# Optimization experiments

Measured on AMD Instinct MI355X. Metric: run time of the kernel, lower is better.

## Reference

```python
import math
import jax, jax.numpy as jnp
import numpy as np

B, C_IN, C_OUT, D_LATENT, H, W, K = 16, 512, 512, 512, 64, 64, 3
EPS = 1e-8


def setup_inputs() -> dict:
    key = jax.random.key(0)
    ks = jax.random.split(key, 6)
    return {
        "x": jax.random.normal(ks[0], (B, C_IN, H, W), dtype=jnp.float32),
        "w": jax.random.normal(ks[1], (B, D_LATENT), dtype=jnp.float32),
        "noise": jax.random.normal(ks[2], (B, 1, H, W), dtype=jnp.float32),
        "style_w": jax.random.normal(ks[3], (C_IN, D_LATENT), dtype=jnp.float32),
        "style_b": jnp.ones((C_IN,), dtype=jnp.float32),  # bias=1.0 in to_style
        "conv_w": jax.random.normal(ks[4], (C_OUT, C_IN, K, K), dtype=jnp.float32),
        "scale_noise": jax.random.normal(ks[5], (1,), dtype=jnp.float32),
        "bias": jnp.zeros((C_OUT,), dtype=jnp.float32),
    }


def reference(x, w, noise, style_w, style_b, conv_w, scale_noise, bias):
    b, c, h, ww = x.shape
    o, _, k, _ = conv_w.shape
    # EqualizedLinear to_style: runtime_coef = 1/sqrt(d_latent), lr_mul=1
    lin_coef = 1.0 / math.sqrt(style_w.shape[1])
    style = w @ (style_w * lin_coef).T + style_b  # [B, C_in]
    # EqualizedWeight for conv: runtime_coef = 1/sqrt(C_in*K*K)
    conv_coef = 1.0 / math.sqrt(c * k * k)
    weights = (conv_w * conv_coef)[None] * style[:, None, :, None, None]  # [B,O,I,K,K]
    # demodulate
    sigma_inv = jax.lax.rsqrt(jnp.sum(weights * weights, axis=(2, 3, 4), keepdims=True) + EPS)
    weights = weights * sigma_inv
    # grouped conv: groups = batch
    xg = x.reshape(1, b * c, h, ww)
    wg = weights.reshape(b * o, c, k, k)
    y = jax.lax.conv_general_dilated(
        xg, wg, window_strides=(1, 1), padding="SAME",
        feature_group_count=b,
        dimension_numbers=("NCHW", "OIHW", "NCHW"))
    y = y.reshape(b, o, h, ww)
    y = y + scale_noise[None, :, None, None] * noise
    return jax.nn.leaky_relu(y + bias[None, :, None, None], negative_slope=0.2)
```

## Files before the change

kernel.cpp:

```cpp
#include <hip/hip_runtime.h>
#include <hip/hip_bf16.h>


#define B_    16
#define CIN   512
#define COUT  512
#define DLAT  512
#define H_    64
#define W_    64

constexpr float LIN_COEF  = 0.04419417382415922f;
constexpr float CONV_COEF = 0.014731391274719739f;

typedef __attribute__((ext_vector_type(8))) short short8;
typedef __attribute__((ext_vector_type(4))) float f32x4;

__device__ __forceinline__ void gl2lds16(const void* g, void* l) {
  __builtin_amdgcn_global_load_lds(
      (const __attribute__((address_space(1))) unsigned*)g,
      (__attribute__((address_space(3))) unsigned*)l, 16, 0, 0);
}

__global__ __launch_bounds__(256) void pre1(
    const float* __restrict__ w, const float* __restrict__ style_w,
    const float* __restrict__ style_b, const float* __restrict__ conv_w,
    float* __restrict__ style, float* __restrict__ wsq,
    __hip_bfloat16* __restrict__ wtp2, __hip_bfloat16* __restrict__ xt) {
  __shared__ float lw[CIN * 9];
  const int bid = blockIdx.x, tid = threadIdx.x;
  if (bid < 2048) {
    int gw = bid * 4 + (tid >> 6), lane = tid & 63;
    int b = gw >> 9, c = gw & 511;
    const float* wp = w + b * DLAT;
    const float* sw = style_w + c * DLAT;
    float v = 0.f;
    for (int d = lane; d < DLAT; d += 64) v = fmaf(wp[d], sw[d], v);
    #pragma unroll
    for (int off = 32; off > 0; off >>= 1) v += __shfl_down(v, off, 64);
    if (lane == 0) style[b * CIN + c] = fmaf(v, LIN_COEF, style_b[c]);
  } else if (bid < 3072) {
    int idx = (bid - 2048) * 256 + tid;
    const float* p = conv_w + (size_t)idx * 9;
    float s = 0.f;
    #pragma unroll
    for (int t = 0; t < 9; ++t) s = fmaf(p[t], p[t], s);
    wsq[idx] = s;
  } else if (bid < 3584) {
    int o = bid - 3072;
    for (int j = tid; j < CIN * 9; j += 256) lw[j] = conv_w[(size_t)o * (CIN * 9) + j];
    __syncthreads();
    for (int g = tid; g < 576; g += 256) {
      int chunk = g / 36, rem = g - chunk * 36, pos = rem >> 2, kqq = rem & 3;
      short8 v;
      #pragma unroll
      for (int e = 0; e < 8; ++e) {
        int ic = chunk * 32 + kqq * 8 + e;
        ((__hip_bfloat16*)&v)[e] = __float2bfloat16(lw[ic * 9 + pos]);
      }
      ((short8*)wtp2)[(size_t)g * 512 + o] = v;
    }
  } else {
    int idx = bid - 3584;
    int b = idx / 260, pb = idx - b * 260;
    int hh, ww;
    if (pb < 66)       { hh = 0;  ww = pb; }
    else if (pb < 132) { hh = 65; ww = pb - 66; }
    else if (pb < 196) { hh = pb - 132 + 1; ww = 0; }
    else               { hh = pb - 196 + 1; ww = 65; }
    unsigned* p = (unsigned*)(xt + (((size_t)b * 66 + hh) * 66 + ww) * CIN);
    p[tid] = 0u;
  }
}

#define LSTR 136
__global__ __launch_bounds__(256) void pre2(
    const float* __restrict__ x, const float* __restrict__ style,
    const float* __restrict__ wsq, float* __restrict__ scale_bo,
    __hip_bfloat16* __restrict__ xt) {
  __shared__ __align__(16) char sm2[64 * LSTR * 2];
  const int bid = blockIdx.x, tid = threadIdx.x;
  if (bid < 2048) {
    int gw = bid * 4 + (tid >> 6), lane = tid & 63;
    int b = gw >> 9, o = gw & 511;
    const float* st = style + b * CIN;
    const float* wq = wsq + o * CIN;
    float v = 0.f;
    for (int i = lane; i < CIN; i += 64) { float s = st[i]; v = fmaf(s * s, wq[i], v); }
    #pragma unroll
    for (int off = 32; off > 0; off >>= 1) v += __shfl_down(v, off, 64);
    if (lane == 0)
      scale_bo[b * COUT + o] = CONV_COEF * rsqrtf(fmaf(CONV_COEF * CONV_COEF, v, 1e-8f));
  } else {
    int idx = bid - 2048;
    int b = idx >> 8, rem = idx & 255, h = rem >> 2, ic0 = (rem & 3) * 128;
    __hip_bfloat16* ls = (__hip_bfloat16*)sm2;
    for (int j = tid; j < 128 * 64; j += 256) {
      int i = j >> 6, ww = j & 63;
      float v = x[(((size_t)b * CIN + ic0 + i) * H_ + h) * W_ + ww] * style[b * CIN + ic0 + i];
      ls[ww * LSTR + i] = __float2bfloat16(v);
    }
    __syncthreads();
    for (int j = tid; j < 64 * 16; j += 256) {
      int ww = j >> 4, part = j & 15;
      __hip_bfloat16* dst = xt + (((size_t)b * 66 + h + 1) * 66 + (ww + 1)) * CIN + ic0 + part * 8;
      *(short8*)dst = *(const short8*)(ls + ww * LSTR + part * 8);
    }
  }
}

__global__ __launch_bounds__(256, 3) void conv_mfma(
    const __hip_bfloat16* __restrict__ xt, const __hip_bfloat16* __restrict__ wtp2,
    const float* __restrict__ scale_bo, const float* __restrict__ noise,
    const float* __restrict__ scale_noise, const float* __restrict__ bias,
    float* __restrict__ out) {
  __shared__ __align__(16) char smem[25344];

  const int tid = threadIdx.x, lane = tid & 63, wid = tid >> 6;
  const int mrow = lane & 15, kq = lane >> 4;
  const int b  = blockIdx.x >> 4;
  const int h0 = (blockIdx.x & 15) << 2;
  const int o0 = blockIdx.y << 6;
  const int h  = h0 + wid;

  const size_t xbase = ((size_t)(b * 66 + h0)) * (66 * 512);
  int xoff[7];
  #pragma unroll
  for (int i = 0; i < 7; ++i) {
    int slot = wid + i * 4;
    int t = slot * 64 + lane;
    if (t < 1584) {
      int p = t >> 2, s = t & 3;
      int q = s ^ ((p >> 1) & 3);
      xoff[i] = p * 512 + q * 8;
    } else xoff[i] = -1;
  }

  f32x4 acc[4][4] = {};
  int pbase[4];
  #pragma unroll
  for (int ms = 0; ms < 4; ++ms) pbase[ms] = wid * 66 + ms * 16 + mrow;

  const short8* bbase = (const short8*)wtp2 + (kq * 512 + o0 + mrow);

  for (int ic0 = 0; ic0 < CIN; ic0 += 32) {
    __syncthreads();
    #pragma unroll
    for (int i = 0; i < 7; ++i)
      if (xoff[i] >= 0)
        gl2lds16(xt + xbase + xoff[i] + ic0, smem + (wid + i * 4) * 1024);
    __syncthreads();

    const int ch9 = (ic0 >> 5) * 9;
    #pragma unroll
    for (int ky = 0; ky < 3; ++ky) {
      #pragma unroll
      for (int kx = 0; kx < 3; ++kx) {
        const short8* bp = bbase + (size_t)(ch9 + ky * 3 + kx) * 2048;
        short8 bf0 = bp[0], bf1 = bp[16], bf2 = bp[32], bf3 = bp[48];
        short8 af[4];
        #pragma unroll
        for (int ms = 0; ms < 4; ++ms) {
          int p = pbase[ms] + ky * 66 + kx;
          int s = kq ^ ((p >> 1) & 3);
          af[ms] = *(const short8*)(smem + p * 64 + s * 16);
        }
        #pragma unroll
        for (int ms = 0; ms < 4; ++ms) {
          acc[ms][0] = __builtin_amdgcn_mfma_f32_16x16x32_bf16(af[ms], bf0, acc[ms][0], 0, 0, 0);
          acc[ms][1] = __builtin_amdgcn_mfma_f32_16x16x32_bf16(af[ms], bf1, acc[ms][1], 0, 0, 0);
          acc[ms][2] = __builtin_amdgcn_mfma_f32_16x16x32_bf16(af[ms], bf2, acc[ms][2], 0, 0, 0);
          acc[ms][3] = __builtin_amdgcn_mfma_f32_16x16x32_bf16(af[ms], bf3, acc[ms][3], 0, 0, 0);
        }
      }
    }
  }

  __syncthreads();
  float* ep = (float*)smem + wid * 1088;
  const float sn = scale_noise[0];
  const float nz = sn * noise[((size_t)b * H_ + h) * W_ + lane];

  for (int ns = 0; ns < 4; ++ns) {
    #pragma unroll
    for (int ms = 0; ms < 4; ++ms) {
      int prow = ms * 16 + kq * 4;
      #pragma unroll
      for (int rg = 0; rg < 4; ++rg)
        ep[(prow + rg) * 17 + mrow] = acc[ms][ns][rg];
    }
    #pragma unroll
    for (int oo = 0; oo < 16; ++oo) {
      int o = o0 + ns * 16 + oo;
      float v = ep[lane * 17 + oo];
      v = fmaf(v, scale_bo[b * COUT + o], nz + bias[o]);
      v = v > 0.f ? v : 0.2f * v;
      out[(((size_t)b * COUT + o) * H_ + h) * W_ + lane] = v;
    }
  }
}

__global__ __launch_bounds__(256) void style_kernel(
    const float* __restrict__ w, const float* __restrict__ style_w,
    const float* __restrict__ style_b, float* __restrict__ style) {
  int gw = blockIdx.x * 4 + (threadIdx.x >> 6);
  int lane = threadIdx.x & 63;
  int b = gw >> 9, c = gw & 511;
  const float* wp = w + b * DLAT;
  const float* sw = style_w + c * DLAT;
  float v = 0.f;
  for (int d = lane; d < DLAT; d += 64) v = fmaf(wp[d], sw[d], v);
  #pragma unroll
  for (int off = 32; off > 0; off >>= 1) v += __shfl_down(v, off, 64);
  if (lane == 0) style[b * CIN + c] = fmaf(v, LIN_COEF, style_b[c]);
}
__global__ __launch_bounds__(256) void wsq_kernel(
    const float* __restrict__ conv_w, float* __restrict__ wsq) {
  int idx = blockIdx.x * 256 + threadIdx.x;
  const float* p = conv_w + (size_t)idx * 9;
  float s = 0.f;
  #pragma unroll
  for (int t = 0; t < 9; ++t) s = fmaf(p[t], p[t], s);
  wsq[idx] = s;
}
__global__ __launch_bounds__(256) void scale_kernel(
    const float* __restrict__ style, const float* __restrict__ wsq,
    float* __restrict__ scale_bo) {
  int gw = blockIdx.x * 4 + (threadIdx.x >> 6);
  int lane = threadIdx.x & 63;
  int b = gw >> 9, o = gw & 511;
  const float* st = style + b * CIN;
  const float* wq = wsq + o * CIN;
  float v = 0.f;
  for (int i = lane; i < CIN; i += 64) { float s = st[i]; v = fmaf(s * s, wq[i], v); }
  #pragma unroll
  for (int off = 32; off > 0; off >>= 1) v += __shfl_down(v, off, 64);
  if (lane == 0)
    scale_bo[b * COUT + o] = CONV_COEF * rsqrtf(fmaf(CONV_COEF * CONV_COEF, v, 1e-8f));
}
#define OTILE 32
#define HTILE 8
#define ICCH  8
#define XSTR  67
#define XROWS 10
__global__ __launch_bounds__(256) void conv_kernel(
    const float* __restrict__ x, const float* __restrict__ style,
    const float* __restrict__ conv_w, const float* __restrict__ scale_bo,
    const float* __restrict__ noise, const float* __restrict__ scale_noise,
    const float* __restrict__ bias, float* __restrict__ out) {
  __shared__ float xtile[ICCH * XROWS * XSTR];
  __shared__ float wt[OTILE * 72];
  const int tid = threadIdx.x;
  const int b = blockIdx.z, o0 = blockIdx.y * OTILE, h0 = blockIdx.x * HTILE;
  const int lane = tid & 63, oq = tid >> 6;
  const int r = lane >> 3, cg = lane & 7;
  float acc[8][8];
  #pragma unroll
  for (int a = 0; a < 8; ++a)
    #pragma unroll
    for (int c = 0; c < 8; ++c) acc[a][c] = 0.f;
  for (int ic0 = 0; ic0 < CIN; ic0 += ICCH) {
    for (int j = tid; j < ICCH * XROWS * XSTR; j += 256) {
      int i = j / (XROWS * XSTR);
      int rem = j - i * (XROWS * XSTR);
      int rr = rem / XSTR, cl = rem - rr * XSTR;
      if (cl < 66) {
        int hh = h0 - 1 + rr, wc = cl - 1;
        float v = 0.f;
        if ((unsigned)hh < 64u && (unsigned)wc < 64u)
          v = x[((size_t)(b * CIN + ic0 + i) * H_ + hh) * W_ + wc] * style[b * CIN + ic0 + i];
        xtile[j] = v;
      }
    }
    for (int j = tid; j < OTILE * 72; j += 256) {
      int oo = j / 72, q = j - oo * 72;
      wt[j] = conv_w[(size_t)(o0 + oo) * (CIN * 9) + ic0 * 9 + q];
    }
    __syncthreads();
    #pragma unroll 1
    for (int i = 0; i < ICCH; ++i) {
      const float* xbi = &xtile[i * (XROWS * XSTR) + r * XSTR + cg * 8];
      const float* wbi = &wt[oq * 8 * 72 + i * 9];
      #pragma unroll
      for (int ky = 0; ky < 3; ++ky) {
        float xr[10];
        #pragma unroll
        for (int q = 0; q < 10; ++q) xr[q] = xbi[ky * XSTR + q];
        #pragma unroll
        for (int kx = 0; kx < 3; ++kx) {
          #pragma unroll
          for (int oo = 0; oo < 8; ++oo) {
            float wv = wbi[oo * 72 + ky * 3 + kx];
            #pragma unroll
            for (int c = 0; c < 8; ++c) acc[oo][c] = fmaf(xr[c + kx], wv, acc[oo][c]);
          }
        }
      }
    }
    __syncthreads();
  }
  const float sn = scale_noise[0];
  const int row = h0 + r;
  float nz[8];
  #pragma unroll
  for (int c = 0; c < 8; ++c)
    nz[c] = sn * noise[((size_t)b * H_ + row) * W_ + cg * 8 + c];
  #pragma unroll
  for (int oo = 0; oo < 8; ++oo) {
    int o = o0 + oq * 8 + oo;
    float s = scale_bo[b * COUT + o];
    float bv = bias[o];
    float* op = out + ((size_t)(b * COUT + o) * H_ + row) * W_ + cg * 8;
    #pragma unroll
    for (int c = 0; c < 8; ++c) {
      float v = fmaf(acc[oo][c], s, nz[c] + bv);
      op[c] = v > 0.f ? v : 0.2f * v;
    }
  }
}

extern "C" void kernel_launch(void* const* d_in, const int* in_sizes, int n_in,
                              void* d_out, int out_size, void* d_ws, size_t ws_size,
                              hipStream_t stream) {
  const float* x           = (const float*)d_in[0];
  const float* w           = (const float*)d_in[1];
  const float* noise       = (const float*)d_in[2];
  const float* style_w     = (const float*)d_in[3];
  const float* style_b     = (const float*)d_in[4];
  const float* conv_w      = (const float*)d_in[5];
  const float* scale_noise = (const float*)d_in[6];
  const float* bias        = (const float*)d_in[7];
  float* out = (float*)d_out;

  float* wsf      = (float*)d_ws;
  float* style    = wsf;
  float* scale_bo = wsf + 8192;
  float* wsq      = wsf + 16384;
  const size_t WTP_OFF = 1114112;
  const size_t XT_OFF  = WTP_OFF + (size_t)COUT * 9 * CIN * 2;
  const size_t NEED    = XT_OFF + (size_t)B_ * 66 * 66 * CIN * 2;

  if (ws_size >= NEED) {
    __hip_bfloat16* wtp2 = (__hip_bfloat16*)((char*)d_ws + WTP_OFF);
    __hip_bfloat16* xtp  = (__hip_bfloat16*)((char*)d_ws + XT_OFF);
    pre1<<<3584 + 16 * 260, 256, 0, stream>>>(w, style_w, style_b, conv_w,
                                              style, wsq, wtp2, xtp);
    pre2<<<2048 + 4096, 256, 0, stream>>>(x, style, wsq, scale_bo, xtp);
    dim3 grid(256, 8, 1);
    conv_mfma<<<grid, 256, 0, stream>>>(xtp, wtp2, scale_bo, noise,
                                        scale_noise, bias, out);
  } else {
    style_kernel<<<2048, 256, 0, stream>>>(w, style_w, style_b, style);
    wsq_kernel<<<1024, 256, 0, stream>>>(conv_w, wsq);
    scale_kernel<<<2048, 256, 0, stream>>>(style, wsq, scale_bo);
    dim3 grid(H_ / HTILE, COUT / OTILE, B_);
    conv_kernel<<<grid, 256, 0, stream>>>(x, style, conv_w, scale_bo,
                                          noise, scale_noise, bias, out);
  }
}
```

Baseline: 540.7 us.

## Double conv tile rows per block, rebalance prep kernels, vectorize x loads

The MFMA conv block now covers 8 output rows instead of 4, and each wave computes two rows with 8 M-subtiles. Every weight fragment loaded from global memory is reused across twice as many MFMAs, and the staging overhead of the halo rows is spread over more output. The cost is a larger LDS tile, a larger accumulator, and occupancy lowered to 2 blocks per CU with half as many blocks. The weight transpose and padding-zero work move from pre1 to pre2 so pre1 is lighter, and the x*style staging now reads float4 vectors.

```diff
diff --git a/kernel.cpp b/kernel.cpp
--- a/kernel.cpp
+++ b/kernel.cpp
@@ -24,9 +24,7 @@
 __global__ __launch_bounds__(256) void pre1(
     const float* __restrict__ w, const float* __restrict__ style_w,
     const float* __restrict__ style_b, const float* __restrict__ conv_w,
-    float* __restrict__ style, float* __restrict__ wsq,
-    __hip_bfloat16* __restrict__ wtp2, __hip_bfloat16* __restrict__ xt) {
-  __shared__ float lw[CIN * 9];
+    float* __restrict__ style, float* __restrict__ wsq) {
   const int bid = blockIdx.x, tid = threadIdx.x;
   if (bid < 2048) {
     int gw = bid * 4 + (tid >> 6), lane = tid & 63;
@@ -38,15 +36,38 @@
     #pragma unroll
     for (int off = 32; off > 0; off >>= 1) v += __shfl_down(v, off, 64);
     if (lane == 0) style[b * CIN + c] = fmaf(v, LIN_COEF, style_b[c]);
-  } else if (bid < 3072) {
+  } else {
     int idx = (bid - 2048) * 256 + tid;
     const float* p = conv_w + (size_t)idx * 9;
     float s = 0.f;
     #pragma unroll
     for (int t = 0; t < 9; ++t) s = fmaf(p[t], p[t], s);
     wsq[idx] = s;
-  } else if (bid < 3584) {
-    int o = bid - 3072;
+  }
+}
+
+#define LSTR 136
+__global__ __launch_bounds__(256) void pre2(
+    const float* __restrict__ x, const float* __restrict__ style,
+    const float* __restrict__ wsq, const float* __restrict__ conv_w,
+    float* __restrict__ scale_bo, __hip_bfloat16* __restrict__ wtp2,
+    __hip_bfloat16* __restrict__ xt) {
+  __shared__ __align__(16) char sm2[18432];
+  const int bid = blockIdx.x, tid = threadIdx.x;
+  if (bid < 2048) {
+    int gw = bid * 4 + (tid >> 6), lane = tid & 63;
+    int b = gw >> 9, o = gw & 511;
+    const float* st = style + b * CIN;
+    const float* wq = wsq + o * CIN;
+    float v = 0.f;
+    for (int i = lane; i < CIN; i += 64) { float s = st[i]; v = fmaf(s * s, wq[i], v); }
+    #pragma unroll
+    for (int off = 32; off > 0; off >>= 1) v += __shfl_down(v, off, 64);
+    if (lane == 0)
+      scale_bo[b * COUT + o] = CONV_COEF * rsqrtf(fmaf(CONV_COEF * CONV_COEF, v, 1e-8f));
+  } else if (bid < 2560) {
+    int o = bid - 2048;
+    float* lw = (float*)sm2;
     for (int j = tid; j < CIN * 9; j += 256) lw[j] = conv_w[(size_t)o * (CIN * 9) + j];
     __syncthreads();
     for (int g = tid; g < 576; g += 256) {
@@ -59,8 +80,8 @@
       }
       ((short8*)wtp2)[(size_t)g * 512 + o] = v;
     }
-  } else {
-    int idx = bid - 3584;
+  } else if (bid < 6720) {
+    int idx = bid - 2560;
     int b = idx / 260, pb = idx - b * 260;
     int hh, ww;
     if (pb < 66)       { hh = 0;  ww = pb; }
@@ -69,38 +90,21 @@
     else               { hh = pb - 196 + 1; ww = 65; }
     unsigned* p = (unsigned*)(xt + (((size_t)b * 66 + hh) * 66 + ww) * CIN);
     p[tid] = 0u;
-  }
-}
-
-#define LSTR 136
-__global__ __launch_bounds__(256) void pre2(
-    const float* __restrict__ x, const float* __restrict__ style,
-    const float* __restrict__ wsq, float* __restrict__ scale_bo,
-    __hip_bfloat16* __restrict__ xt) {
-  __shared__ __align__(16) char sm2[64 * LSTR * 2];
-  const int bid = blockIdx.x, tid = threadIdx.x;
-  if (bid < 2048) {
-    int gw = bid * 4 + (tid >> 6), lane = tid & 63;
-    int b = gw >> 9, o = gw & 511;
-    const float* st = style + b * CIN;
-    const float* wq = wsq + o * CIN;
-    float v = 0.f;
-    for (int i = lane; i < CIN; i += 64) { float s = st[i]; v = fmaf(s * s, wq[i], v); }
-    #pragma unroll
-    for (int off = 32; off > 0; off >>= 1) v += __shfl_down(v, off, 64);
-    if (lane == 0)
-      scale_bo[b * COUT + o] = CONV_COEF * rsqrtf(fmaf(CONV_COEF * CONV_COEF, v, 1e-8f));
   } else {
-    int idx = bid - 2048;
+    int idx = bid - 6720;
     int b = idx >> 8, rem = idx & 255, h = rem >> 2, ic0 = (rem & 3) * 128;
     __hip_bfloat16* ls = (__hip_bfloat16*)sm2;
-    for (int j = tid; j < 128 * 64; j += 256) {
-      int i = j >> 6, ww = j & 63;
-      float v = x[(((size_t)b * CIN + ic0 + i) * H_ + h) * W_ + ww] * style[b * CIN + ic0 + i];
-      ls[ww * LSTR + i] = __float2bfloat16(v);
-    }
-    __syncthreads();
-    for (int j = tid; j < 64 * 16; j += 256) {
+    for (int j = tid; j < 2048; j += 256) {
+      int i = j >> 4, wq = j & 15;
+      const float4 xv = *(const float4*)&x[(((size_t)b * CIN + ic0 + i) * H_ + h) * W_ + wq * 4];
+      float st = style[b * CIN + ic0 + i];
+      ls[(wq * 4 + 0) * LSTR + i] = __float2bfloat16(xv.x * st);
+      ls[(wq * 4 + 1) * LSTR + i] = __float2bfloat16(xv.y * st);
+      ls[(wq * 4 + 2) * LSTR + i] = __float2bfloat16(xv.z * st);
+      ls[(wq * 4 + 3) * LSTR + i] = __float2bfloat16(xv.w * st);
+    }
+    __syncthreads();
+    for (int j = tid; j < 1024; j += 256) {
       int ww = j >> 4, part = j & 15;
       __hip_bfloat16* dst = xt + (((size_t)b * 66 + h + 1) * 66 + (ww + 1)) * CIN + ic0 + part * 8;
       *(short8*)dst = *(const short8*)(ls + ww * LSTR + part * 8);
@@ -108,44 +112,45 @@
   }
 }
 
-__global__ __launch_bounds__(256, 3) void conv_mfma(
+__global__ __launch_bounds__(256, 2) void conv_mfma(
     const __hip_bfloat16* __restrict__ xt, const __hip_bfloat16* __restrict__ wtp2,
     const float* __restrict__ scale_bo, const float* __restrict__ noise,
     const float* __restrict__ scale_noise, const float* __restrict__ bias,
     float* __restrict__ out) {
-  __shared__ __align__(16) char smem[25344];
+  __shared__ __align__(16) char smem[42240];
 
   const int tid = threadIdx.x, lane = tid & 63, wid = tid >> 6;
   const int mrow = lane & 15, kq = lane >> 4;
-  const int b  = blockIdx.x >> 4;
-  const int h0 = (blockIdx.x & 15) << 2;
+  const int b  = blockIdx.x >> 3;
+  const int h0 = (blockIdx.x & 7) << 3;
   const int o0 = blockIdx.y << 6;
-  const int h  = h0 + wid;
+  const int r0 = h0 + (wid << 1);
 
   const size_t xbase = ((size_t)(b * 66 + h0)) * (66 * 512);
-  int xoff[7];
-  #pragma unroll
-  for (int i = 0; i < 7; ++i) {
+  int xoff[11];
+  #pragma unroll
+  for (int i = 0; i < 11; ++i) {
     int slot = wid + i * 4;
     int t = slot * 64 + lane;
-    if (t < 1584) {
+    if (t < 2640) {
       int p = t >> 2, s = t & 3;
       int q = s ^ ((p >> 1) & 3);
       xoff[i] = p * 512 + q * 8;
     } else xoff[i] = -1;
   }
 
-  f32x4 acc[4][4] = {};
-  int pbase[4];
-  #pragma unroll
-  for (int ms = 0; ms < 4; ++ms) pbase[ms] = wid * 66 + ms * 16 + mrow;
+  f32x4 acc[8][4] = {};
+  int pbase[8];
+  #pragma unroll
+  for (int ms = 0; ms < 8; ++ms)
+    pbase[ms] = ((wid << 1) + (ms >> 2)) * 66 + (ms & 3) * 16 + mrow;
 
   const short8* bbase = (const short8*)wtp2 + (kq * 512 + o0 + mrow);
 
   for (int ic0 = 0; ic0 < CIN; ic0 += 32) {
     __syncthreads();
     #pragma unroll
-    for (int i = 0; i < 7; ++i)
+    for (int i = 0; i < 11; ++i)
       if (xoff[i] >= 0)
         gl2lds16(xt + xbase + xoff[i] + ic0, smem + (wid + i * 4) * 1024);
     __syncthreads();
@@ -157,15 +162,15 @@
       for (int kx = 0; kx < 3; ++kx) {
         const short8* bp = bbase + (size_t)(ch9 + ky * 3 + kx) * 2048;
         short8 bf0 = bp[0], bf1 = bp[16], bf2 = bp[32], bf3 = bp[48];
-        short8 af[4];
-        #pragma unroll
-        for (int ms = 0; ms < 4; ++ms) {
+        short8 af[8];
+        #pragma unroll
+        for (int ms = 0; ms < 8; ++ms) {
           int p = pbase[ms] + ky * 66 + kx;
           int s = kq ^ ((p >> 1) & 3);
           af[ms] = *(const short8*)(smem + p * 64 + s * 16);
         }
         #pragma unroll
-        for (int ms = 0; ms < 4; ++ms) {
+        for (int ms = 0; ms < 8; ++ms) {
           acc[ms][0] = __builtin_amdgcn_mfma_f32_16x16x32_bf16(af[ms], bf0, acc[ms][0], 0, 0, 0);
           acc[ms][1] = __builtin_amdgcn_mfma_f32_16x16x32_bf16(af[ms], bf1, acc[ms][1], 0, 0, 0);
           acc[ms][2] = __builtin_amdgcn_mfma_f32_16x16x32_bf16(af[ms], bf2, acc[ms][2], 0, 0, 0);
@@ -178,23 +183,28 @@
   __syncthreads();
   float* ep = (float*)smem + wid * 1088;
   const float sn = scale_noise[0];
-  const float nz = sn * noise[((size_t)b * H_ + h) * W_ + lane];
-
-  for (int ns = 0; ns < 4; ++ns) {
-    #pragma unroll
-    for (int ms = 0; ms < 4; ++ms) {
-      int prow = ms * 16 + kq * 4;
-      #pragma unroll
-      for (int rg = 0; rg < 4; ++rg)
-        ep[(prow + rg) * 17 + mrow] = acc[ms][ns][rg];
-    }
-    #pragma unroll
-    for (int oo = 0; oo < 16; ++oo) {
-      int o = o0 + ns * 16 + oo;
-      float v = ep[lane * 17 + oo];
-      v = fmaf(v, scale_bo[b * COUT + o], nz + bias[o]);
-      v = v > 0.f ? v : 0.2f * v;
-      out[(((size_t)b * COUT + o) * H_ + h) * W_ + lane] = v;
+
+  #pragma unroll
+  for (int r = 0; r < 2; ++r) {
+    const int h = r0 + r;
+    const float nz = sn * noise[((size_t)b * H_ + h) * W_ + lane];
+    for (int ns = 0; ns < 4; ++ns) {
+      #pragma unroll
+      for (int m4 = 0; m4 < 4; ++m4) {
+        int ms = r * 4 + m4;
+        int prow = m4 * 16 + kq * 4;
+        #pragma unroll
+        for (int rg = 0; rg < 4; ++rg)
+          ep[(prow + rg) * 17 + mrow] = acc[ms][ns][rg];
+      }
+      #pragma unroll
+      for (int oo = 0; oo < 16; ++oo) {
+        int o = o0 + ns * 16 + oo;
+        float v = ep[lane * 17 + oo];
+        v = fmaf(v, scale_bo[b * COUT + o], nz + bias[o]);
+        v = v > 0.f ? v : 0.2f * v;
+        out[(((size_t)b * COUT + o) * H_ + h) * W_ + lane] = v;
+      }
     }
   }
 }
@@ -342,10 +352,9 @@
   if (ws_size >= NEED) {
     __hip_bfloat16* wtp2 = (__hip_bfloat16*)((char*)d_ws + WTP_OFF);
     __hip_bfloat16* xtp  = (__hip_bfloat16*)((char*)d_ws + XT_OFF);
-    pre1<<<3584 + 16 * 260, 256, 0, stream>>>(w, style_w, style_b, conv_w,
-                                              style, wsq, wtp2, xtp);
-    pre2<<<2048 + 4096, 256, 0, stream>>>(x, style, wsq, scale_bo, xtp);
-    dim3 grid(256, 8, 1);
+    pre1<<<3072, 256, 0, stream>>>(w, style_w, style_b, conv_w, style, wsq);
+    pre2<<<10816, 256, 0, stream>>>(x, style, wsq, conv_w, scale_bo, wtp2, xtp);
+    dim3 grid(128, 8, 1);
     conv_mfma<<<grid, 256, 0, stream>>>(xtp, wtp2, scale_bo, noise,
                                         scale_noise, bias, out);
   } else {
```

Result: faster. 529.5 us (-2.1%).
